# Performance work log

Hardware: AMD Instinct MI355X
Metric: run time of the kernel (lower is better)

Reference implementation:

```python
import jax, jax.numpy as jnp
import numpy as np

S, B, D, H = 2048, 2, 1024, 16
DK = D // H  # 64

def setup_inputs() -> dict:
    key0 = jax.random.key(0)
    ks = jax.random.split(key0, 11)
    scale = 0.02
    inp = {
        'query': jax.random.normal(ks[0], (S, B, D), jnp.float32),
        'key':   jax.random.normal(ks[1], (S, B, D), jnp.float32),
        'value': jax.random.normal(ks[2], (S, B, D), jnp.float32),
        # nn.Linear weights stored torch-style [out_features, in_features]
        'Wq': jax.random.normal(ks[3], (H * DK, D), jnp.float32) * scale,
        'bq': jnp.zeros((H * DK,), jnp.float32),
        'Wk': jax.random.normal(ks[4], (H * DK, D), jnp.float32) * scale,
        'bk': jnp.zeros((H * DK,), jnp.float32),
        'Wv': jax.random.normal(ks[5], (H * DK, D), jnp.float32) * scale,
        'bv': jnp.zeros((H * DK,), jnp.float32),
        'Wo': jax.random.normal(ks[6], (D, D), jnp.float32) * scale,
        'bo': jnp.zeros((D,), jnp.float32),
    }
    return inp

def _proj(x, W, b):
    # x: [S,B,D] -> [S,B,H,DK]
    y = jnp.einsum('sbd,ed->sbe', x, W) + b
    return y.reshape(x.shape[0], x.shape[1], H, DK)

def reference(query, key, value, Wq, bq, Wk, bk, Wv, bv, Wo, bo):
    q = _proj(query, Wq, bq)   # [S,B,H,DK]
    k = _proj(key,   Wk, bk)
    v = _proj(value, Wv, bv)
    # NOTE: original forward never applies self.scale -> unscaled QK^T (faithful)
    scores = jnp.einsum('ibhd,jbhd->ijbh', q, k)      # [Sq,Sk,B,H]
    attn = jax.nn.softmax(scores, axis=1)             # softmax over key axis j
    x = jnp.einsum('ijbh,jbhd->ibhd', attn, v)        # [S,B,H,DK]
    x = x.reshape(q.shape[0], q.shape[1], H * DK)     # [S,B,D]
    out = jnp.einsum('sbd,ed->sbe', x, Wo) + bo       # [S,B,D]
    return out
```

## Files before the change

kernel.cpp:

```cpp
#include <hip/hip_runtime.h>
#include <stdint.h>

#define S_LEN  2048
#define BATCH  2
#define DMODEL 1024
#define NHEAD  16
#define DKH    64

typedef __attribute__((ext_vector_type(8))) __bf16 bf16x8;
typedef __attribute__((ext_vector_type(4))) float  f32x4;
typedef unsigned short u16;
typedef unsigned int   u32;

__device__ __forceinline__ u16 f2bf(float f) {
  union { float f; u32 u; } v; v.f = f;
  u32 r = v.u + 0x7fffu + ((v.u >> 16) & 1u);
  return (u16)(r >> 16);
}

__global__ void cvt3_kernel(const float4* __restrict__ a, const float4* __restrict__ b,
                            const float4* __restrict__ c,
                            ushort4* __restrict__ oa, ushort4* __restrict__ ob,
                            ushort4* __restrict__ oc, int n4) {
  int i = blockIdx.x * blockDim.x + threadIdx.x;
  if (i >= n4) return;
  const float4* src = (blockIdx.y == 0) ? a : (blockIdx.y == 1) ? b : c;
  ushort4*      dst = (blockIdx.y == 0) ? oa : (blockIdx.y == 1) ? ob : oc;
  float4 v = src[i];
  ushort4 o;
  o.x = f2bf(v.x); o.y = f2bf(v.y); o.z = f2bf(v.z); o.w = f2bf(v.w);
  dst[i] = o;
}

__global__ void cvt4_kernel(const float4* __restrict__ a, const float4* __restrict__ b,
                            const float4* __restrict__ c, const float4* __restrict__ d,
                            ushort4* __restrict__ oa, ushort4* __restrict__ ob,
                            ushort4* __restrict__ oc, ushort4* __restrict__ od, int n4) {
  int i = blockIdx.x * blockDim.x + threadIdx.x;
  if (i >= n4) return;
  const float4* src = (blockIdx.y == 0) ? a : (blockIdx.y == 1) ? b : (blockIdx.y == 2) ? c : d;
  ushort4*      dst = (blockIdx.y == 0) ? oa : (blockIdx.y == 1) ? ob : (blockIdx.y == 2) ? oc : od;
  float4 v = src[i];
  ushort4 o;
  o.x = f2bf(v.x); o.y = f2bf(v.y); o.z = f2bf(v.z); o.w = f2bf(v.w);
  dst[i] = o;
}

__global__ __launch_bounds__(256, 2)
void gemm_qkv(const u16* __restrict__ Abase, const u16* __restrict__ Wbase,
              const float* __restrict__ b0, const float* __restrict__ b1,
              const float* __restrict__ b2, u16* __restrict__ Obase) {
  __shared__ __align__(16) u16 As[128 * 32];
  __shared__ __align__(16) u16 Bs[128 * 32];

  const int z = blockIdx.z;
  const u16* A = Abase + (size_t)z * (S_LEN * BATCH * DMODEL);
  const u16* W = Wbase + (size_t)z * (DMODEL * DMODEL);
  const float* bias = (z == 0) ? b0 : (z == 1) ? b1 : b2;
  u16* O = Obase + (size_t)z * (S_LEN * BATCH * DMODEL);

  const int tid  = threadIdx.x;
  const int wave = tid >> 6, lane = tid & 63;
  const int quad = lane >> 4, lcol = lane & 15;
  const int m0 = blockIdx.y * 128, n0 = blockIdx.x * 128;
  const int wm = (wave >> 1) * 64, wn = (wave & 1) * 64;

  f32x4 acc[4][4] = {};

  for (int k0 = 0; k0 < DMODEL; k0 += 32) {
#pragma unroll
    for (int r = 0; r < 2; ++r) {
      int idx = r * 256 + tid;
      int row = idx >> 2, col = (idx & 3) * 8;
      const u16* gA = A + (size_t)(m0 + row) * DMODEL + k0 + col;
      const u16* gW = W + (size_t)(n0 + row) * DMODEL + k0 + col;
      u16* lA = As + (size_t)(r * 256 + (tid & 192)) * 8;
      u16* lB = Bs + (size_t)(r * 256 + (tid & 192)) * 8;
      __builtin_amdgcn_global_load_lds((const __attribute__((address_space(1))) void*)gA,
                                       (__attribute__((address_space(3))) void*)lA, 16, 0, 0);
      __builtin_amdgcn_global_load_lds((const __attribute__((address_space(1))) void*)gW,
                                       (__attribute__((address_space(3))) void*)lB, 16, 0, 0);
    }
    __syncthreads();

    const u16* aBase = As + (wm + lcol) * 32 + quad * 8;
    const u16* bBase = Bs + (wn + lcol) * 32 + quad * 8;
    bf16x8 af[4], bfr[4];
#pragma unroll
    for (int i = 0; i < 4; ++i) af[i]  = *(const bf16x8*)(aBase + i * 16 * 32);
#pragma unroll
    for (int j = 0; j < 4; ++j) bfr[j] = *(const bf16x8*)(bBase + j * 16 * 32);
#pragma unroll
    for (int i = 0; i < 4; ++i)
#pragma unroll
      for (int j = 0; j < 4; ++j)
        acc[i][j] = __builtin_amdgcn_mfma_f32_16x16x32_bf16(af[i], bfr[j], acc[i][j], 0, 0, 0);
    __syncthreads();
  }

#pragma unroll
  for (int i = 0; i < 4; ++i) {
#pragma unroll
    for (int j = 0; j < 4; ++j) {
      int n = n0 + wn + j * 16 + lcol;
      int h = n >> 6, dk = n & 63;
      float bv = bias[n];
#pragma unroll
      for (int r = 0; r < 4; ++r) {
        int m = m0 + wm + i * 16 + quad * 4 + r;
        int s = m >> 1, b = m & 1;
        O[((size_t)(b * NHEAD + h) * S_LEN + s) * DKH + dk] = f2bf(acc[i][j][r] + bv);
      }
    }
  }
}

__global__ __launch_bounds__(256, 2)
void gemm_o(const u16* __restrict__ A, const u16* __restrict__ W,
            const float* __restrict__ bias, float* __restrict__ O) {
  __shared__ __align__(16) u16 As[128 * 32];
  __shared__ __align__(16) u16 Bs[64 * 32];

  const int tid  = threadIdx.x;
  const int wave = tid >> 6, lane = tid & 63;
  const int quad = lane >> 4, lcol = lane & 15;
  const int m0 = blockIdx.y * 128, n0 = blockIdx.x * 64;
  const int wm = (wave >> 1) * 64, wn = (wave & 1) * 32;

  f32x4 acc[4][2] = {};

  for (int k0 = 0; k0 < DMODEL; k0 += 32) {
#pragma unroll
    for (int r = 0; r < 2; ++r) {
      int idx = r * 256 + tid;
      int row = idx >> 2, col = (idx & 3) * 8;
      const u16* gA = A + (size_t)(m0 + row) * DMODEL + k0 + col;
      u16* lA = As + (size_t)(r * 256 + (tid & 192)) * 8;
      __builtin_amdgcn_global_load_lds((const __attribute__((address_space(1))) void*)gA,
                                       (__attribute__((address_space(3))) void*)lA, 16, 0, 0);
    }
    {
      int row = tid >> 2, col = (tid & 3) * 8;
      const u16* gW = W + (size_t)(n0 + row) * DMODEL + k0 + col;
      u16* lB = Bs + (size_t)(tid & 192) * 8;
      __builtin_amdgcn_global_load_lds((const __attribute__((address_space(1))) void*)gW,
                                       (__attribute__((address_space(3))) void*)lB, 16, 0, 0);
    }
    __syncthreads();

    const u16* aBase = As + (wm + lcol) * 32 + quad * 8;
    const u16* bBase = Bs + (wn + lcol) * 32 + quad * 8;
    bf16x8 af[4], bfr[2];
#pragma unroll
    for (int i = 0; i < 4; ++i) af[i]  = *(const bf16x8*)(aBase + i * 16 * 32);
#pragma unroll
    for (int j = 0; j < 2; ++j) bfr[j] = *(const bf16x8*)(bBase + j * 16 * 32);
#pragma unroll
    for (int i = 0; i < 4; ++i)
#pragma unroll
      for (int j = 0; j < 2; ++j)
        acc[i][j] = __builtin_amdgcn_mfma_f32_16x16x32_bf16(af[i], bfr[j], acc[i][j], 0, 0, 0);
    __syncthreads();
  }

#pragma unroll
  for (int i = 0; i < 4; ++i) {
#pragma unroll
    for (int j = 0; j < 2; ++j) {
      int n = n0 + wn + j * 16 + lcol;
      float bv = bias[n];
#pragma unroll
      for (int r = 0; r < 4; ++r) {
        int m = m0 + wm + i * 16 + quad * 4 + r;
        O[(size_t)m * DMODEL + n] = acc[i][j][r] + bv;
      }
    }
  }
}

__global__ __launch_bounds__(256, 3)
void attn_kernel(const u16* __restrict__ Q, const u16* __restrict__ K,
                 const u16* __restrict__ V, u16* __restrict__ O) {
  __shared__ __align__(16) u16 Ks[64 * 72];
  __shared__ __align__(16) u16 Vts[64 * 72];
  __shared__ __align__(16) u16 Ps[4][32 * 72];
  __shared__ float l_s[128];

  const int tid  = threadIdx.x;
  const int wave = tid >> 6, lane = tid & 63;
  const int quad = lane >> 4, lcol = lane & 15;
  const int bh = blockIdx.y;
  const int q0 = blockIdx.x * 128;

  const size_t headOff = (size_t)bh * S_LEN * DKH;
  const u16* Qg = Q + headOff;
  const u16* Kg = K + headOff;
  const u16* Vg = V + headOff;

  bf16x8 qf[2][2];
#pragma unroll
  for (int s = 0; s < 2; ++s)
#pragma unroll
    for (int ks = 0; ks < 2; ++ks)
      qf[s][ks] = *(const bf16x8*)(Qg + (size_t)(q0 + wave * 32 + s * 16 + lcol) * DKH +
                                   ks * 32 + quad * 8);

  f32x4 o_acc[2][4] = {};
  float lsum[2] = {0.f, 0.f};

  const int vkp = tid & 31;
  const int vo  = tid >> 5;

  for (int kt = 0; kt < S_LEN; kt += 64) {
    __syncthreads();
#pragma unroll
    for (int r = 0; r < 2; ++r) {
      int idx = r * 256 + tid;
      int row = idx >> 3, c0 = (idx & 7) * 8;
      *(uint4*)(Ks + row * 72 + c0) = *(const uint4*)(Kg + (size_t)(kt + row) * DKH + c0);
    }
    {
      const u16* vp = Vg + (size_t)(kt + 2 * vkp) * DKH + 8 * vo;
      uint4 va = *(const uint4*)vp;
      uint4 vb = *(const uint4*)(vp + DKH);
      const u16* pa = (const u16*)&va;
      const u16* pb = (const u16*)&vb;
#pragma unroll
      for (int jj = 0; jj < 8; ++jj) {
        u32 w = (u32)pa[jj] | ((u32)pb[jj] << 16);
        *(u32*)(Vts + (size_t)(8 * vo + jj) * 72 + 2 * vkp) = w;
      }
    }
    __syncthreads();

    f32x4 sc[2][4] = {};
#pragma unroll
    for (int ks = 0; ks < 2; ++ks) {
      bf16x8 ak[4];
#pragma unroll
      for (int j = 0; j < 4; ++j)
        ak[j] = *(const bf16x8*)(Ks + (j * 16 + lcol) * 72 + ks * 32 + quad * 8);
#pragma unroll
      for (int s = 0; s < 2; ++s)
#pragma unroll
        for (int j = 0; j < 4; ++j)
          sc[s][j] = __builtin_amdgcn_mfma_f32_16x16x32_bf16(ak[j], qf[s][ks], sc[s][j], 0, 0, 0);
    }

#pragma unroll
    for (int s = 0; s < 2; ++s) {
      u16* prow = Ps[wave] + (s * 16 + lcol) * 72;
#pragma unroll
      for (int j = 0; j < 4; ++j) {
        float p0 = __expf(sc[s][j][0]);
        float p1 = __expf(sc[s][j][1]);
        float p2 = __expf(sc[s][j][2]);
        float p3 = __expf(sc[s][j][3]);
        lsum[s] += (p0 + p1) + (p2 + p3);
        u32 w0 = (u32)f2bf(p0) | ((u32)f2bf(p1) << 16);
        u32 w1 = (u32)f2bf(p2) | ((u32)f2bf(p3) << 16);
        uint2 pk; pk.x = w0; pk.y = w1;
        *(uint2*)(prow + j * 16 + quad * 4) = pk;
      }
    }

#pragma unroll
    for (int ks = 0; ks < 2; ++ks) {
      bf16x8 bv[4];
#pragma unroll
      for (int jd = 0; jd < 4; ++jd)
        bv[jd] = *(const bf16x8*)(Vts + (jd * 16 + lcol) * 72 + ks * 32 + quad * 8);
#pragma unroll
      for (int s = 0; s < 2; ++s) {
        bf16x8 ap = *(const bf16x8*)(Ps[wave] + (s * 16 + lcol) * 72 + ks * 32 + quad * 8);
#pragma unroll
        for (int jd = 0; jd < 4; ++jd)
          o_acc[s][jd] = __builtin_amdgcn_mfma_f32_16x16x32_bf16(ap, bv[jd], o_acc[s][jd], 0, 0, 0);
      }
    }
  }

#pragma unroll
  for (int s = 0; s < 2; ++s) {
    lsum[s] += __shfl_xor(lsum[s], 16);
    lsum[s] += __shfl_xor(lsum[s], 32);
  }
  if (lane < 16) {
    l_s[wave * 32 + lane]      = lsum[0];
    l_s[wave * 32 + 16 + lane] = lsum[1];
  }
  __syncthreads();

  const int b = bh >> 4, h = bh & 15;
#pragma unroll
  for (int s = 0; s < 2; ++s) {
#pragma unroll
    for (int r = 0; r < 4; ++r) {
      float inv = 1.f / l_s[wave * 32 + s * 16 + quad * 4 + r];
      int sq = q0 + wave * 32 + s * 16 + quad * 4 + r;
#pragma unroll
      for (int jd = 0; jd < 4; ++jd) {
        int dk = jd * 16 + lcol;
        O[((size_t)(sq * BATCH + b)) * DMODEL + h * DKH + dk] = f2bf(o_acc[s][jd][r] * inv);
      }
    }
  }
}

extern "C" void kernel_launch(void* const* d_in, const int* in_sizes, int n_in,
                              void* d_out, int out_size, void* d_ws, size_t ws_size,
                              hipStream_t stream) {
  const float* q  = (const float*)d_in[0];
  const float* k  = (const float*)d_in[1];
  const float* v  = (const float*)d_in[2];
  const float* Wq = (const float*)d_in[3];
  const float* bq = (const float*)d_in[4];
  const float* Wk = (const float*)d_in[5];
  const float* bk = (const float*)d_in[6];
  const float* Wv = (const float*)d_in[7];
  const float* bv = (const float*)d_in[8];
  const float* Wo = (const float*)d_in[9];
  const float* bo = (const float*)d_in[10];

  const int NX = S_LEN * BATCH * DMODEL;
  const int NW = DMODEL * DMODEL;

  u16* ws  = (u16*)d_ws;
  u16* Xq  = ws;
  u16* Wqb = Xq  + 3 * (size_t)NX;
  u16* Qb  = Wqb + 4 * (size_t)NW;
  u16* Xo  = Qb  + 3 * (size_t)NX;

  u16* Xk  = Xq + NX, *Xv = Xq + 2 * (size_t)NX;
  u16* Wkb = Wqb + NW, *Wvb = Wqb + 2 * (size_t)NW, *Wob = Wqb + 3 * (size_t)NW;
  u16* Kb  = Qb + NX, *Vb = Qb + 2 * (size_t)NX;

  dim3 g3(NX / 4 / 256, 3);
  cvt3_kernel<<<g3, 256, 0, stream>>>((const float4*)q, (const float4*)k, (const float4*)v,
                                      (ushort4*)Xq, (ushort4*)Xk, (ushort4*)Xv, NX / 4);
  dim3 g4(NW / 4 / 256, 4);
  cvt4_kernel<<<g4, 256, 0, stream>>>((const float4*)Wq, (const float4*)Wk, (const float4*)Wv,
                                      (const float4*)Wo,
                                      (ushort4*)Wqb, (ushort4*)Wkb, (ushort4*)Wvb, (ushort4*)Wob,
                                      NW / 4);

  dim3 gqkv(DMODEL / 128, (S_LEN * BATCH) / 128, 3);
  gemm_qkv<<<gqkv, 256, 0, stream>>>(Xq, Wqb, bq, bk, bv, Qb);

  dim3 ga(S_LEN / 128, BATCH * NHEAD);
  attn_kernel<<<ga, 256, 0, stream>>>(Qb, Kb, Vb, Xo);

  dim3 go(DMODEL / 64, (S_LEN * BATCH) / 128);
  gemm_o<<<go, 256, 0, stream>>>(Xo, Wob, bo, (float*)d_out);
}
```

Before: 249.7 us.

## Double-buffer K/V tiles in attention and fold log2e into Q for exp2

The attention loop now double-buffers K and V^T in shared memory, prefetching the next tile into registers before the compute and writing it to the other buffer afterwards, so each iteration needs one barrier instead of two. Q is pre-scaled by log2(e) in the QKV projection epilogue so the softmax can use the hardware exp2, and packed bf16 conversion plus byte-perm transposes replace the manual rounding. MFMA sections are wrapped in s_setprio. The larger LDS footprint and prefetch registers lower the occupancy hint from 3 to 2 blocks, and the v_cvt_pk_bf16_f32 conversion may round differently from the old manual round-to-nearest-even.

```diff
diff --git a/kernel.cpp b/kernel.cpp
--- a/kernel.cpp
+++ b/kernel.cpp
@@ -11,6 +11,12 @@
 typedef __attribute__((ext_vector_type(4))) float  f32x4;
 typedef unsigned short u16;
 typedef unsigned int   u32;
+
+#if __has_builtin(__builtin_amdgcn_exp2f)
+#define EXP2(x) __builtin_amdgcn_exp2f(x)
+#else
+#define EXP2(x) __expf(0.69314718055994531f * (x))
+#endif
 
 __device__ __forceinline__ u16 f2bf(float f) {
   union { float f; u32 u; } v; v.f = f;
@@ -58,6 +64,7 @@
   const u16* W = Wbase + (size_t)z * (DMODEL * DMODEL);
   const float* bias = (z == 0) ? b0 : (z == 1) ? b1 : b2;
   u16* O = Obase + (size_t)z * (S_LEN * BATCH * DMODEL);
+  const float scl = (z == 0) ? 1.4426950408889634f : 1.0f;
 
   const int tid  = threadIdx.x;
   const int wave = tid >> 6, lane = tid & 63;
@@ -109,7 +116,7 @@
       for (int r = 0; r < 4; ++r) {
         int m = m0 + wm + i * 16 + quad * 4 + r;
         int s = m >> 1, b = m & 1;
-        O[((size_t)(b * NHEAD + h) * S_LEN + s) * DKH + dk] = f2bf(acc[i][j][r] + bv);
+        O[((size_t)(b * NHEAD + h) * S_LEN + s) * DKH + dk] = f2bf((acc[i][j][r] + bv) * scl);
       }
     }
   }
@@ -178,11 +185,11 @@
   }
 }
 
-__global__ __launch_bounds__(256, 3)
+__global__ __launch_bounds__(256, 2)
 void attn_kernel(const u16* __restrict__ Q, const u16* __restrict__ K,
                  const u16* __restrict__ V, u16* __restrict__ O) {
-  __shared__ __align__(16) u16 Ks[64 * 72];
-  __shared__ __align__(16) u16 Vts[64 * 72];
+  __shared__ __align__(16) u16 Ks[2][64 * 72];
+  __shared__ __align__(16) u16 Vts[2][64 * 72];
   __shared__ __align__(16) u16 Ps[4][32 * 72];
   __shared__ float l_s[128];
 
@@ -205,33 +212,46 @@
       qf[s][ks] = *(const bf16x8*)(Qg + (size_t)(q0 + wave * 32 + s * 16 + lcol) * DKH +
                                    ks * 32 + quad * 8);
 
+  const int vkp  = tid & 31;
+  const int vo   = tid >> 5;
+  const int krow = tid >> 3, kc0 = (tid & 7) * 8;
+
+  {
+    uint4 k0 = *(const uint4*)(Kg + (size_t)krow * DKH + kc0);
+    uint4 k1 = *(const uint4*)(Kg + (size_t)(32 + krow) * DKH + kc0);
+    const u16* vp = Vg + (size_t)(2 * vkp) * DKH + 8 * vo;
+    uint4 a = *(const uint4*)vp;
+    uint4 b = *(const uint4*)(vp + DKH);
+    *(uint4*)(Ks[0] + krow * 72 + kc0)        = k0;
+    *(uint4*)(Ks[0] + (32 + krow) * 72 + kc0) = k1;
+#pragma unroll
+    for (int w = 0; w < 4; ++w) {
+      u32 aw = ((const u32*)&a)[w], bw = ((const u32*)&b)[w];
+      *(u32*)(Vts[0] + (size_t)(8 * vo + 2 * w) * 72 + 2 * vkp)     = __builtin_amdgcn_perm(bw, aw, 0x05040100u);
+      *(u32*)(Vts[0] + (size_t)(8 * vo + 2 * w + 1) * 72 + 2 * vkp) = __builtin_amdgcn_perm(bw, aw, 0x07060302u);
+    }
+  }
+
   f32x4 o_acc[2][4] = {};
   float lsum[2] = {0.f, 0.f};
 
-  const int vkp = tid & 31;
-  const int vo  = tid >> 5;
-
-  for (int kt = 0; kt < S_LEN; kt += 64) {
-    __syncthreads();
-#pragma unroll
-    for (int r = 0; r < 2; ++r) {
-      int idx = r * 256 + tid;
-      int row = idx >> 3, c0 = (idx & 7) * 8;
-      *(uint4*)(Ks + row * 72 + c0) = *(const uint4*)(Kg + (size_t)(kt + row) * DKH + c0);
-    }
-    {
-      const u16* vp = Vg + (size_t)(kt + 2 * vkp) * DKH + 8 * vo;
-      uint4 va = *(const uint4*)vp;
-      uint4 vb = *(const uint4*)(vp + DKH);
-      const u16* pa = (const u16*)&va;
-      const u16* pb = (const u16*)&vb;
-#pragma unroll
-      for (int jj = 0; jj < 8; ++jj) {
-        u32 w = (u32)pa[jj] | ((u32)pb[jj] << 16);
-        *(u32*)(Vts + (size_t)(8 * vo + jj) * 72 + 2 * vkp) = w;
-      }
-    }
-    __syncthreads();
+  for (int it = 0; it < S_LEN / 64; ++it) {
+    const int cur = it & 1;
+    const int ktn = (it + 1) * 64;
+    const bool has = (ktn < S_LEN);
+
+    uint4 nk0, nk1, nva, nvb;
+    if (has) {
+      nk0 = *(const uint4*)(Kg + (size_t)(ktn + krow) * DKH + kc0);
+      nk1 = *(const uint4*)(Kg + (size_t)(ktn + 32 + krow) * DKH + kc0);
+      const u16* vp = Vg + (size_t)(ktn + 2 * vkp) * DKH + 8 * vo;
+      nva = *(const uint4*)vp;
+      nvb = *(const uint4*)(vp + DKH);
+    }
+    __syncthreads();
+
+    const u16* ksrc = Ks[cur];
+    const u16* vsrc = Vts[cur];
 
     f32x4 sc[2][4] = {};
 #pragma unroll
@@ -239,12 +259,14 @@
       bf16x8 ak[4];
 #pragma unroll
       for (int j = 0; j < 4; ++j)
-        ak[j] = *(const bf16x8*)(Ks + (j * 16 + lcol) * 72 + ks * 32 + quad * 8);
+        ak[j] = *(const bf16x8*)(ksrc + (j * 16 + lcol) * 72 + ks * 32 + quad * 8);
+      __builtin_amdgcn_s_setprio(1);
 #pragma unroll
       for (int s = 0; s < 2; ++s)
 #pragma unroll
         for (int j = 0; j < 4; ++j)
           sc[s][j] = __builtin_amdgcn_mfma_f32_16x16x32_bf16(ak[j], qf[s][ks], sc[s][j], 0, 0, 0);
+      __builtin_amdgcn_s_setprio(0);
     }
 
 #pragma unroll
@@ -252,13 +274,14 @@
       u16* prow = Ps[wave] + (s * 16 + lcol) * 72;
 #pragma unroll
       for (int j = 0; j < 4; ++j) {
-        float p0 = __expf(sc[s][j][0]);
-        float p1 = __expf(sc[s][j][1]);
-        float p2 = __expf(sc[s][j][2]);
-        float p3 = __expf(sc[s][j][3]);
+        float p0 = EXP2(sc[s][j][0]);
+        float p1 = EXP2(sc[s][j][1]);
+        float p2 = EXP2(sc[s][j][2]);
+        float p3 = EXP2(sc[s][j][3]);
         lsum[s] += (p0 + p1) + (p2 + p3);
-        u32 w0 = (u32)f2bf(p0) | ((u32)f2bf(p1) << 16);
-        u32 w1 = (u32)f2bf(p2) | ((u32)f2bf(p3) << 16);
+        u32 w0, w1;
+        asm("v_cvt_pk_bf16_f32 %0, %1, %2" : "=v"(w0) : "v"(p0), "v"(p1));
+        asm("v_cvt_pk_bf16_f32 %0, %1, %2" : "=v"(w1) : "v"(p2), "v"(p3));
         uint2 pk; pk.x = w0; pk.y = w1;
         *(uint2*)(prow + j * 16 + quad * 4) = pk;
       }
@@ -269,13 +292,28 @@
       bf16x8 bv[4];
 #pragma unroll
       for (int jd = 0; jd < 4; ++jd)
-        bv[jd] = *(const bf16x8*)(Vts + (jd * 16 + lcol) * 72 + ks * 32 + quad * 8);
+        bv[jd] = *(const bf16x8*)(vsrc + (jd * 16 + lcol) * 72 + ks * 32 + quad * 8);
+      __builtin_amdgcn_s_setprio(1);
 #pragma unroll
       for (int s = 0; s < 2; ++s) {
         bf16x8 ap = *(const bf16x8*)(Ps[wave] + (s * 16 + lcol) * 72 + ks * 32 + quad * 8);
 #pragma unroll
         for (int jd = 0; jd < 4; ++jd)
           o_acc[s][jd] = __builtin_amdgcn_mfma_f32_16x16x32_bf16(ap, bv[jd], o_acc[s][jd], 0, 0, 0);
+      }
+      __builtin_amdgcn_s_setprio(0);
+    }
+
+    if (has) {
+      u16* kdst = Ks[cur ^ 1];
+      u16* vdst = Vts[cur ^ 1];
+      *(uint4*)(kdst + krow * 72 + kc0)        = nk0;
+      *(uint4*)(kdst + (32 + krow) * 72 + kc0) = nk1;
+#pragma unroll
+      for (int w = 0; w < 4; ++w) {
+        u32 aw = ((const u32*)&nva)[w], bw = ((const u32*)&nvb)[w];
+        *(u32*)(vdst + (size_t)(8 * vo + 2 * w) * 72 + 2 * vkp)     = __builtin_amdgcn_perm(bw, aw, 0x05040100u);
+        *(u32*)(vdst + (size_t)(8 * vo + 2 * w + 1) * 72 + 2 * vkp) = __builtin_amdgcn_perm(bw, aw, 0x07060302u);
       }
     }
   }
```

Measured after the change: 226.1 us. 1.1x faster.

## Split attention keys across two wave groups, keep P in registers, prefetch K/V

Applied to the files above, without the earlier changes.

The attention kernel now runs 512 threads, with two groups of four waves each handling half of the key sequence for the same 128 queries. Partial outputs and row sums are combined through shared memory at the end. The P tile stays in registers, using permlane swaps and packed bf16 conversion instead of a shared-memory round trip. K/V tiles for the next step are prefetched into registers, and MFMA sections get raised priority. Q is pre-scaled by log2(e) in the QKV GEMM so exp2 can replace exp, which keeps results equivalent but adds register pressure and a cross-group reduction.

```diff
diff --git a/kernel.cpp b/kernel.cpp
--- a/kernel.cpp
+++ b/kernel.cpp
@@ -11,6 +11,15 @@
 typedef __attribute__((ext_vector_type(4))) float  f32x4;
 typedef unsigned short u16;
 typedef unsigned int   u32;
+
+#if __has_builtin(__builtin_amdgcn_exp2f)
+#define EXP2(x) __builtin_amdgcn_exp2f(x)
+#else
+#define EXP2(x) __expf(0.69314718055994531f * (x))
+#endif
+
+#define SWAP32(a, b) asm("v_permlane32_swap_b32 %0, %1" : "+v"(a), "+v"(b))
+#define SWAP16(a, b) asm("v_permlane16_swap_b32 %0, %1" : "+v"(a), "+v"(b))
 
 __device__ __forceinline__ u16 f2bf(float f) {
   union { float f; u32 u; } v; v.f = f;
@@ -58,6 +67,7 @@
   const u16* W = Wbase + (size_t)z * (DMODEL * DMODEL);
   const float* bias = (z == 0) ? b0 : (z == 1) ? b1 : b2;
   u16* O = Obase + (size_t)z * (S_LEN * BATCH * DMODEL);
+  const float scl = (z == 0) ? 1.4426950408889634f : 1.0f;
 
   const int tid  = threadIdx.x;
   const int wave = tid >> 6, lane = tid & 63;
@@ -109,7 +119,7 @@
       for (int r = 0; r < 4; ++r) {
         int m = m0 + wm + i * 16 + quad * 4 + r;
         int s = m >> 1, b = m & 1;
-        O[((size_t)(b * NHEAD + h) * S_LEN + s) * DKH + dk] = f2bf(acc[i][j][r] + bv);
+        O[((size_t)(b * NHEAD + h) * S_LEN + s) * DKH + dk] = f2bf((acc[i][j][r] + bv) * scl);
       }
     }
   }
@@ -178,17 +188,19 @@
   }
 }
 
-__global__ __launch_bounds__(256, 3)
+__global__ __launch_bounds__(512, 4)
 void attn_kernel(const u16* __restrict__ Q, const u16* __restrict__ K,
                  const u16* __restrict__ V, u16* __restrict__ O) {
-  __shared__ __align__(16) u16 Ks[64 * 72];
-  __shared__ __align__(16) u16 Vts[64 * 72];
-  __shared__ __align__(16) u16 Ps[4][32 * 72];
-  __shared__ float l_s[128];
+  __shared__ __align__(16) u16 smem[2 * 4608 + 2 * 4608];
+  __shared__ float l_s2[4][32];
+  u16* Ks  = smem;
+  u16* Vts = smem + 2 * 4608;
 
   const int tid  = threadIdx.x;
   const int wave = tid >> 6, lane = tid & 63;
   const int quad = lane >> 4, lcol = lane & 15;
+  const int h  = wave >> 2;
+  const int qw = wave & 3;
   const int bh = blockIdx.y;
   const int q0 = blockIdx.x * 128;
 
@@ -202,36 +214,50 @@
   for (int s = 0; s < 2; ++s)
 #pragma unroll
     for (int ks = 0; ks < 2; ++ks)
-      qf[s][ks] = *(const bf16x8*)(Qg + (size_t)(q0 + wave * 32 + s * 16 + lcol) * DKH +
+      qf[s][ks] = *(const bf16x8*)(Qg + (size_t)(q0 + qw * 32 + s * 16 + lcol) * DKH +
                                    ks * 32 + quad * 8);
+
+  const int krow  = tid >> 3, kch = tid & 7;
+  const int vhalf = (lane >> 5), vkp = lane & 31;
+  const int vo    = wave;
+
+  uint4 kr0 = *(const uint4*)(Kg + (size_t)krow * DKH + kch * 8);
+  uint4 kr1 = *(const uint4*)(Kg + (size_t)(S_LEN / 2 + krow) * DKH + kch * 8);
+  uint4 vr0, vr1;
+  {
+    const u16* vp = Vg + (size_t)(vhalf * (S_LEN / 2) + 2 * vkp) * DKH + 8 * vo;
+    vr0 = *(const uint4*)vp;
+    vr1 = *(const uint4*)(vp + DKH);
+  }
 
   f32x4 o_acc[2][4] = {};
   float lsum[2] = {0.f, 0.f};
 
-  const int vkp = tid & 31;
-  const int vo  = tid >> 5;
-
-  for (int kt = 0; kt < S_LEN; kt += 64) {
-    __syncthreads();
-#pragma unroll
-    for (int r = 0; r < 2; ++r) {
-      int idx = r * 256 + tid;
-      int row = idx >> 3, c0 = (idx & 7) * 8;
-      *(uint4*)(Ks + row * 72 + c0) = *(const uint4*)(Kg + (size_t)(kt + row) * DKH + c0);
-    }
+  for (int it = 0; it < 16; ++it) {
+    *(uint4*)(Ks + (size_t)krow * 72 + kch * 8)        = kr0;
+    *(uint4*)(Ks + (size_t)(64 + krow) * 72 + kch * 8) = kr1;
     {
-      const u16* vp = Vg + (size_t)(kt + 2 * vkp) * DKH + 8 * vo;
-      uint4 va = *(const uint4*)vp;
-      uint4 vb = *(const uint4*)(vp + DKH);
-      const u16* pa = (const u16*)&va;
-      const u16* pb = (const u16*)&vb;
-#pragma unroll
-      for (int jj = 0; jj < 8; ++jj) {
-        u32 w = (u32)pa[jj] | ((u32)pb[jj] << 16);
-        *(u32*)(Vts + (size_t)(8 * vo + jj) * 72 + 2 * vkp) = w;
-      }
-    }
-    __syncthreads();
+      u16* vd = Vts + vhalf * 4608;
+#pragma unroll
+      for (int jj = 0; jj < 4; ++jj) {
+        u32 aw = ((const u32*)&vr0)[jj], bw = ((const u32*)&vr1)[jj];
+        *(u32*)(vd + (size_t)(8 * vo + 2 * jj) * 72 + 2 * vkp)     = __builtin_amdgcn_perm(bw, aw, 0x05040100u);
+        *(u32*)(vd + (size_t)(8 * vo + 2 * jj + 1) * 72 + 2 * vkp) = __builtin_amdgcn_perm(bw, aw, 0x07060302u);
+      }
+    }
+    __syncthreads();
+
+    if (it < 15) {
+      int nb = (it + 1) * 64;
+      kr0 = *(const uint4*)(Kg + (size_t)(nb + krow) * DKH + kch * 8);
+      kr1 = *(const uint4*)(Kg + (size_t)(S_LEN / 2 + nb + krow) * DKH + kch * 8);
+      const u16* vp = Vg + (size_t)(vhalf * (S_LEN / 2) + nb + 2 * vkp) * DKH + 8 * vo;
+      vr0 = *(const uint4*)vp;
+      vr1 = *(const uint4*)(vp + DKH);
+    }
+
+    const u16* kb = Ks  + h * 4608;
+    const u16* vb = Vts + h * 4608;
 
     f32x4 sc[2][4] = {};
 #pragma unroll
@@ -239,28 +265,39 @@
       bf16x8 ak[4];
 #pragma unroll
       for (int j = 0; j < 4; ++j)
-        ak[j] = *(const bf16x8*)(Ks + (j * 16 + lcol) * 72 + ks * 32 + quad * 8);
+        ak[j] = *(const bf16x8*)(kb + (j * 16 + lcol) * 72 + ks * 32 + quad * 8);
+      __builtin_amdgcn_s_setprio(1);
 #pragma unroll
       for (int s = 0; s < 2; ++s)
 #pragma unroll
         for (int j = 0; j < 4; ++j)
           sc[s][j] = __builtin_amdgcn_mfma_f32_16x16x32_bf16(ak[j], qf[s][ks], sc[s][j], 0, 0, 0);
-    }
-
+      __builtin_amdgcn_s_setprio(0);
+    }
+
+    bf16x8 pa[2][2];
 #pragma unroll
     for (int s = 0; s < 2; ++s) {
-      u16* prow = Ps[wave] + (s * 16 + lcol) * 72;
+      u32 ww[4][2];
 #pragma unroll
       for (int j = 0; j < 4; ++j) {
-        float p0 = __expf(sc[s][j][0]);
-        float p1 = __expf(sc[s][j][1]);
-        float p2 = __expf(sc[s][j][2]);
-        float p3 = __expf(sc[s][j][3]);
+        float p0 = EXP2(sc[s][j][0]);
+        float p1 = EXP2(sc[s][j][1]);
+        float p2 = EXP2(sc[s][j][2]);
+        float p3 = EXP2(sc[s][j][3]);
         lsum[s] += (p0 + p1) + (p2 + p3);
-        u32 w0 = (u32)f2bf(p0) | ((u32)f2bf(p1) << 16);
-        u32 w1 = (u32)f2bf(p2) | ((u32)f2bf(p3) << 16);
-        uint2 pk; pk.x = w0; pk.y = w1;
-        *(uint2*)(prow + j * 16 + quad * 4) = pk;
+        asm("v_cvt_pk_bf16_f32 %0, %1, %2" : "=v"(ww[j][0]) : "v"(p0), "v"(p1));
+        asm("v_cvt_pk_bf16_f32 %0, %1, %2" : "=v"(ww[j][1]) : "v"(p2), "v"(p3));
+      }
+#pragma unroll
+      for (int ks = 0; ks < 2; ++ks) {
+        u32 a0 = ww[2 * ks][0], b0 = ww[2 * ks + 1][0];
+        SWAP32(a0, b0); SWAP16(a0, b0);
+        u32 a1 = ww[2 * ks][1], b1 = ww[2 * ks + 1][1];
+        SWAP32(a1, b1); SWAP16(a1, b1);
+        union { u32 u[4]; bf16x8 v; } f;
+        f.u[0] = a0; f.u[1] = a1; f.u[2] = b0; f.u[3] = b1;
+        pa[s][ks] = f.v;
       }
     }
 
@@ -269,15 +306,17 @@
       bf16x8 bv[4];
 #pragma unroll
       for (int jd = 0; jd < 4; ++jd)
-        bv[jd] = *(const bf16x8*)(Vts + (jd * 16 + lcol) * 72 + ks * 32 + quad * 8);
-#pragma unroll
-      for (int s = 0; s < 2; ++s) {
-        bf16x8 ap = *(const bf16x8*)(Ps[wave] + (s * 16 + lcol) * 72 + ks * 32 + quad * 8);
+        bv[jd] = *(const bf16x8*)(vb + (jd * 16 + lcol) * 72 + ks * 32 + quad * 8);
+      __builtin_amdgcn_s_setprio(1);
+#pragma unroll
+      for (int s = 0; s < 2; ++s)
 #pragma unroll
         for (int jd = 0; jd < 4; ++jd)
-          o_acc[s][jd] = __builtin_amdgcn_mfma_f32_16x16x32_bf16(ap, bv[jd], o_acc[s][jd], 0, 0, 0);
-      }
-    }
+          o_acc[s][jd] = __builtin_amdgcn_mfma_f32_16x16x32_bf16(pa[s][ks], bv[jd], o_acc[s][jd], 0, 0, 0);
+      __builtin_amdgcn_s_setprio(0);
+    }
+
+    __syncthreads();
   }
 
 #pragma unroll
@@ -285,23 +324,44 @@
     lsum[s] += __shfl_xor(lsum[s], 16);
     lsum[s] += __shfl_xor(lsum[s], 32);
   }
-  if (lane < 16) {
-    l_s[wave * 32 + lane]      = lsum[0];
-    l_s[wave * 32 + 16 + lane] = lsum[1];
+
+  float* scr = (float*)smem;
+  if (wave >= 4) {
+    int base = ((wave - 4) * 64 + lane) * 36;
+#pragma unroll
+    for (int s = 0; s < 2; ++s)
+#pragma unroll
+      for (int jd = 0; jd < 4; ++jd)
+        *(f32x4*)(scr + base + (s * 4 + jd) * 4) = o_acc[s][jd];
+    if (lane < 16) {
+      l_s2[wave - 4][lane]      = lsum[0];
+      l_s2[wave - 4][16 + lane] = lsum[1];
+    }
   }
   __syncthreads();
-
-  const int b = bh >> 4, h = bh & 15;
-#pragma unroll
-  for (int s = 0; s < 2; ++s) {
-#pragma unroll
-    for (int r = 0; r < 4; ++r) {
-      float inv = 1.f / l_s[wave * 32 + s * 16 + quad * 4 + r];
-      int sq = q0 + wave * 32 + s * 16 + quad * 4 + r;
-#pragma unroll
-      for (int jd = 0; jd < 4; ++jd) {
-        int dk = jd * 16 + lcol;
-        O[((size_t)(sq * BATCH + b)) * DMODEL + h * DKH + dk] = f2bf(o_acc[s][jd][r] * inv);
+  if (wave < 4) {
+    int base = (wave * 64 + lane) * 36;
+#pragma unroll
+    for (int s = 0; s < 2; ++s)
+#pragma unroll
+      for (int jd = 0; jd < 4; ++jd)
+        o_acc[s][jd] += *(const f32x4*)(scr + base + (s * 4 + jd) * 4);
+    float tot0 = lsum[0] + l_s2[wave][lcol];
+    float tot1 = lsum[1] + l_s2[wave][16 + lcol];
+
+    const int b = bh >> 4, hh = bh & 15;
+#pragma unroll
+    for (int s = 0; s < 2; ++s) {
+      float tot = (s == 0) ? tot0 : tot1;
+#pragma unroll
+      for (int r = 0; r < 4; ++r) {
+        float inv = 1.f / __shfl(tot, quad * 4 + r);
+        int sq = q0 + wave * 32 + s * 16 + quad * 4 + r;
+#pragma unroll
+        for (int jd = 0; jd < 4; ++jd) {
+          int dk = jd * 16 + lcol;
+          O[((size_t)(sq * BATCH + b)) * DMODEL + hh * DKH + dk] = f2bf(o_acc[s][jd][r] * inv);
+        }
       }
     }
   }
@@ -348,7 +408,7 @@
   gemm_qkv<<<gqkv, 256, 0, stream>>>(Xq, Wqb, bq, bk, bv, Qb);
 
   dim3 ga(S_LEN / 128, BATCH * NHEAD);
-  attn_kernel<<<ga, 256, 0, stream>>>(Qb, Kb, Vb, Xo);
+  attn_kernel<<<ga, 512, 0, stream>>>(Qb, Kb, Vb, Xo);
 
   dim3 go(DMODEL / 64, (S_LEN * BATCH) / 128);
   gemm_o<<<go, 256, 0, stream>>>(Xo, Wob, bo, (float*)d_out);
```

Measured after the change: 228.0 us. 8.7% less time.
